# Performance work log

Measured on AMD Instinct MI355X. Metric: run time of the kernel, lower is better.

Reference implementation:

```python
import jax, jax.numpy as jnp
import numpy as np

N_NODES = 50000
NUM_HEAD = 2
NEG_SLOPE_ATT = 0.2
NEG_SLOPE_ACT = 0.3


def _glorot(key, shape):
    fan = shape[-1] + (shape[-2] if len(shape) > 1 else shape[-1])
    lim = jnp.sqrt(6.0 / fan)
    return jax.random.uniform(key, shape, jnp.float32, -lim, lim)


def gat_conv(h, src, dst, W, att, bias):
    # h: (N, in_dim); W: (out_dim, in_dim) torch Linear layout; att: (1, H, 2k)
    N = h.shape[0]
    H = att.shape[1]
    k = att.shape[2] // 2
    x = (h @ W.T).reshape(N, H, k)
    x_i = x[dst]  # target features (E, H, k)
    x_j = x[src]  # source features (E, H, k)
    # alpha = sum(cat([x_i, x_j]) * att) without materializing the concat
    alpha = jnp.einsum('ehk,hk->eh', x_i, att[0, :, :k]) + jnp.einsum('ehk,hk->eh', x_j, att[0, :, k:])
    alpha = jax.nn.leaky_relu(alpha, NEG_SLOPE_ATT)
    # segment softmax grouped by edge_index[0] (src), as in the original code
    m = jax.ops.segment_max(alpha, src, num_segments=N)
    e = jnp.exp(alpha - m[src])
    s = jax.ops.segment_sum(e, src, num_segments=N)
    alpha = e / (s[src] + 1e-16)
    msg = x_j * alpha[:, :, None]
    out = jax.ops.segment_sum(msg, dst, num_segments=N)  # aggregate to targets
    out = out.reshape(N, H * k) + bias
    return jax.nn.relu(out)


def _forward(x, src, dst, node_index, params):
    (W1, att1, b1, W2, att2, b2, W3, att3, b3, W_out, b_out) = params
    h = gat_conv(x, src, dst, W1, att1, b1)
    h = jax.nn.leaky_relu(h, NEG_SLOPE_ACT)
    h = gat_conv(h, src, dst, W2, att2, b2)
    h = jax.nn.leaky_relu(h, NEG_SLOPE_ACT)
    h = gat_conv(h, src, dst, W3, att3, b3)
    x_embed = jax.nn.leaky_relu(h, NEG_SLOPE_ACT)
    output = x_embed @ W_out.T + b_out
    node_output = output[node_index]
    ypred = jnp.argmax(output, axis=1)
    y_nodepred = ypred[node_index]
    return x_embed, node_output, ypred, y_nodepred


def setup_inputs() -> dict:
    key = jax.random.key(0)
    ks = jax.random.split(key, 16)
    N, E, D = N_NODES, 800000, 128
    H, k = NUM_HEAD, 128 // NUM_HEAD
    inp = {
        'x': jax.random.normal(ks[0], (N, D), jnp.float32),
        'edge_index': jax.random.randint(ks[1], (2, E), 0, N, jnp.int64),
        'node_label': jax.random.normal(ks[2], (1000, 1, 3), jnp.float32),
        'node_index': jax.random.randint(ks[3], (1000,), 0, N, jnp.int64),
        'W1': _glorot(ks[4], (D, D)),
        'att1': _glorot(ks[5], (1, H, 2 * k)),
        'b1': jnp.zeros((D,), jnp.float32),
        'W2': _glorot(ks[6], (D, D)),
        'att2': _glorot(ks[7], (1, H, 2 * k)),
        'b2': jnp.zeros((D,), jnp.float32),
        'W3': _glorot(ks[8], (D, D)),
        'att3': _glorot(ks[9], (1, H, 2 * k)),
        'b3': jnp.zeros((D,), jnp.float32),
        'W_out': _glorot(ks[10], (3, D)),
        'b_out': jnp.zeros((3,), jnp.float32),
    }
    return inp


def reference(x, edge_index, node_label, node_index, W1, att1, b1, W2, att2, b2, W3, att3, b3, W_out, b_out):
    N = x.shape[0]
    loop = jnp.arange(N, dtype=edge_index.dtype)
    src = jnp.concatenate([edge_index[0], loop])  # add_self_loops
    dst = jnp.concatenate([edge_index[1], loop])
    params = (W1, att1, b1, W2, att2, b2, W3, att3, b3, W_out, b_out)
    return _forward(x, src, dst, node_index, params)
```

## Files before the change

### kernel.cpp

```cpp
#include <hip/hip_runtime.h>
#include <math.h>


#define EPB 8192

__global__ __launch_bounds__(256) void gemm128(const float* __restrict__ A,
                                               const float* __restrict__ Wm,
                                               const float* __restrict__ att,
                                               float* __restrict__ C,
                                               float4* __restrict__ ni4,
                                               float2* __restrict__ ad2v, int N) {
    __shared__ float As[64][68];
    __shared__ float Wt[64][132];
    const int tx = threadIdx.x;
    const int row0 = blockIdx.x * 64;
    const int cid = tx & 31;
    const int rid = tx >> 5;
    float acc[8][4] = {};
    const float4* A4 = (const float4*)A;
    const float4* W4 = (const float4*)Wm;

    for (int kt = 0; kt < 2; ++kt) {
        for (int i = tx; i < 1024; i += 256) {
            int r = i >> 4, q = i & 15;
            int row = row0 + r;
            float4 v = (row < N) ? A4[(size_t)row * 32 + kt * 16 + q]
                                 : make_float4(0.f, 0.f, 0.f, 0.f);
            As[r][q * 4 + 0] = v.x; As[r][q * 4 + 1] = v.y;
            As[r][q * 4 + 2] = v.z; As[r][q * 4 + 3] = v.w;
        }
        for (int i = tx; i < 2048; i += 256) {
            int c = i >> 4, q = i & 15;
            float4 v = W4[(size_t)c * 32 + kt * 16 + q];
            Wt[q * 4 + 0][c] = v.x; Wt[q * 4 + 1][c] = v.y;
            Wt[q * 4 + 2][c] = v.z; Wt[q * 4 + 3][c] = v.w;
        }
        __syncthreads();
        for (int k = 0; k < 64; k += 4) {
            float4 a[8];
            #pragma unroll
            for (int i = 0; i < 8; ++i) a[i] = *(const float4*)&As[rid * 8 + i][k];
            #pragma unroll
            for (int kk = 0; kk < 4; ++kk) {
                float4 w = *(const float4*)&Wt[k + kk][cid * 4];
                #pragma unroll
                for (int i = 0; i < 8; ++i) {
                    float av = (kk == 0) ? a[i].x : (kk == 1) ? a[i].y : (kk == 2) ? a[i].z : a[i].w;
                    acc[i][0] += av * w.x; acc[i][1] += av * w.y;
                    acc[i][2] += av * w.z; acc[i][3] += av * w.w;
                }
            }
        }
        __syncthreads();
    }
    #pragma unroll
    for (int i = 0; i < 8; ++i) {
        int row = row0 + rid * 8 + i;
        if (row < N)
            ((float4*)C)[(size_t)row * 32 + cid] =
                make_float4(acc[i][0], acc[i][1], acc[i][2], acc[i][3]);
    }
    const int hh = cid >> 4;
    const int c0 = (cid & 15) * 4;
    float ad0 = att[hh * 128 + c0 + 0], ad1 = att[hh * 128 + c0 + 1];
    float ad2c = att[hh * 128 + c0 + 2], ad3 = att[hh * 128 + c0 + 3];
    float as0 = att[hh * 128 + 64 + c0 + 0], as1 = att[hh * 128 + 64 + c0 + 1];
    float as2 = att[hh * 128 + 64 + c0 + 2], as3 = att[hh * 128 + 64 + c0 + 3];
    float pd[8], ps[8];
    #pragma unroll
    for (int i = 0; i < 8; ++i) {
        pd[i] = acc[i][0] * ad0 + acc[i][1] * ad1 + acc[i][2] * ad2c + acc[i][3] * ad3;
        ps[i] = acc[i][0] * as0 + acc[i][1] * as1 + acc[i][2] * as2 + acc[i][3] * as3;
    }
    #pragma unroll
    for (int m = 1; m < 16; m <<= 1) {
        #pragma unroll
        for (int i = 0; i < 8; ++i) {
            pd[i] += __shfl_xor(pd[i], m);
            ps[i] += __shfl_xor(ps[i], m);
        }
    }
    const int ll = tx & 63;
    const int grp = ll & 32;
    #pragma unroll
    for (int i = 0; i < 8; ++i) {
        float d0 = __shfl(pd[i], grp + 0);
        float d1 = __shfl(pd[i], grp + 16);
        float s0 = __shfl(ps[i], grp + 0);
        float s1 = __shfl(ps[i], grp + 16);
        if ((ll & 31) == 0) {
            int row = row0 + rid * 8 + i;
            if (row < N) {
                ad2v[row] = make_float2(d0, d1);
                ni4[row] = make_float4(s0, s1, 0.f, 0.f);
            }
        }
    }
}

__global__ __launch_bounds__(512) void coarse_hist(const int* __restrict__ ei, int E, int Et,
                                                   unsigned int* __restrict__ gh_d,
                                                   unsigned int* __restrict__ gh_s, int CB) {
    __shared__ unsigned int lh_d[800];
    __shared__ unsigned int lh_s[800];
    const int t = threadIdx.x;
    for (int b = t; b < CB; b += 512) { lh_d[b] = 0u; lh_s[b] = 0u; }
    __syncthreads();
    const int i0 = blockIdx.x * EPB;
    for (int i = t; i < EPB; i += 512) {
        int e = i0 + i;
        if (e < Et) {
            int s, d;
            if (e < E) { s = ei[e]; d = ei[E + e]; } else { s = d = e - E; }
            atomicAdd(&lh_d[d >> 6], 1u);
            atomicAdd(&lh_s[s >> 6], 1u);
        }
    }
    __syncthreads();
    for (int b = t; b < CB; b += 512) {
        if (lh_d[b]) atomicAdd(&gh_d[b], lh_d[b]);
        if (lh_s[b]) atomicAdd(&gh_s[b], lh_s[b]);
    }
}

__global__ __launch_bounds__(1024) void coarse_scan(const unsigned int* __restrict__ gh_d,
                                                    const unsigned int* __restrict__ gh_s,
                                                    unsigned int* __restrict__ coff_d,
                                                    unsigned int* __restrict__ coff_s,
                                                    unsigned int* __restrict__ cur_d,
                                                    unsigned int* __restrict__ cur_s,
                                                    int CB, unsigned int total) {
    __shared__ unsigned int sh[1024];
    const int t = threadIdx.x;
    for (int a = 0; a < 2; ++a) {
        const unsigned int* gh = a ? gh_s : gh_d;
        unsigned int* coff = a ? coff_s : coff_d;
        unsigned int* cur  = a ? cur_s : cur_d;
        sh[t] = (t < CB) ? gh[t] : 0u;
        __syncthreads();
        #pragma unroll
        for (int d = 1; d < 1024; d <<= 1) {
            unsigned int u = (t >= d) ? sh[t - d] : 0u;
            __syncthreads();
            sh[t] += u;
            __syncthreads();
        }
        if (t < CB) {
            unsigned int ex = (t == 0) ? 0u : sh[t - 1];
            coff[t] = ex;
            cur[t] = ex;
        }
        if (t == 0) coff[CB] = total;
        __syncthreads();
    }
}

__global__ __launch_bounds__(512) void coarse_scatter_both(const int* __restrict__ ei,
                                                           int E, int Et,
                                                           unsigned int* __restrict__ cur_d,
                                                           unsigned int* __restrict__ cur_s,
                                                           unsigned int* __restrict__ tmp_d,
                                                           unsigned int* __restrict__ tmp_s,
                                                           int CB) {
    __shared__ unsigned int lh_d[800];
    __shared__ unsigned int lh_s[800];
    const int t = threadIdx.x;
    for (int b = t; b < CB; b += 512) { lh_d[b] = 0u; lh_s[b] = 0u; }
    __syncthreads();
    const int i0 = blockIdx.x * EPB;
    for (int i = t; i < EPB; i += 512) {
        int e = i0 + i;
        if (e < Et) {
            int s, d;
            if (e < E) { s = ei[e]; d = ei[E + e]; } else { s = d = e - E; }
            atomicAdd(&lh_d[d >> 6], 1u);
            atomicAdd(&lh_s[s >> 6], 1u);
        }
    }
    __syncthreads();
    for (int b = t; b < CB; b += 512) {
        unsigned int cd = lh_d[b], cs = lh_s[b];
        lh_d[b] = cd ? atomicAdd(&cur_d[b], cd) : 0u;
        lh_s[b] = cs ? atomicAdd(&cur_s[b], cs) : 0u;
    }
    __syncthreads();
    for (int i = t; i < EPB; i += 512) {
        int e = i0 + i;
        if (e < Et) {
            int s, d;
            if (e < E) { s = ei[e]; d = ei[E + e]; } else { s = d = e - E; }
            unsigned int pd = atomicAdd(&lh_d[d >> 6], 1u);
            tmp_d[pd] = ((unsigned int)(d & 63) << 16) | (unsigned int)s;
            unsigned int ps = atomicAdd(&lh_s[s >> 6], 1u);
            tmp_s[ps] = ((unsigned int)(s & 63) << 16) | (unsigned int)d;
        }
    }
}

__global__ __launch_bounds__(256) void fine_sort(const unsigned int* __restrict__ tmp_d,
                                                 const unsigned int* __restrict__ tmp_s,
                                                 const unsigned int* __restrict__ coff_d,
                                                 const unsigned int* __restrict__ coff_s,
                                                 unsigned int* __restrict__ off_d,
                                                 unsigned int* __restrict__ off_s,
                                                 int* __restrict__ srcs,
                                                 int* __restrict__ dsts,
                                                 int N, int CB, unsigned int total) {
    __shared__ unsigned int cnt[64];
    __shared__ unsigned int h[64];
    const bool isS = (int)blockIdx.x >= CB;
    const int b = isS ? (blockIdx.x - CB) : blockIdx.x;
    const unsigned int* tmp  = isS ? tmp_s : tmp_d;
    const unsigned int* coff = isS ? coff_s : coff_d;
    unsigned int* off = isS ? off_s : off_d;
    int* outv = isS ? dsts : srcs;
    const int node0 = b * 64;
    int nn = N - node0; if (nn > 64) nn = 64;
    const int t = threadIdx.x;
    const unsigned int cb0 = coff[b], cb1 = coff[b + 1];
    if (t < 64) cnt[t] = 0u;
    __syncthreads();
    for (unsigned int i = cb0 + t; i < cb1; i += 256)
        atomicAdd(&cnt[tmp[i] >> 16], 1u);
    __syncthreads();
    if (t < 64) h[t] = cnt[t];
    __syncthreads();
    #pragma unroll
    for (int d = 1; d < 64; d <<= 1) {
        unsigned int u = (t < 64 && t >= d) ? h[t - d] : 0u;
        __syncthreads();
        if (t < 64) h[t] += u;
        __syncthreads();
    }
    if (t < 64) h[t] = cb0 + h[t] - cnt[t];
    __syncthreads();
    if (t < nn) off[node0 + t] = h[t];
    if (b == CB - 1 && t == 0) off[N] = total;
    for (unsigned int i = cb0 + t; i < cb1; i += 256) {
        unsigned int v = tmp[i];
        unsigned int pos = atomicAdd(&h[v >> 16], 1u);
        outv[pos] = (int)(v & 0xFFFFu);
    }
}

__global__ __launch_bounds__(256) void src_sum(const int* __restrict__ dsts,
                                               const unsigned int* __restrict__ off_s,
                                               const float2* __restrict__ ad2,
                                               float* __restrict__ ni, int N) {
    int n = blockIdx.x * 256 + threadIdx.x;
    if (n >= N) return;
    float as0 = ni[(size_t)n * 4 + 0];
    float as1 = ni[(size_t)n * 4 + 1];
    unsigned int j0 = off_s[n], j1 = off_s[n + 1];
    float s0 = 0.f, s1 = 0.f;
    unsigned int j = j0;
    for (; j + 4 <= j1; j += 4) {
        int d0 = dsts[j], d1 = dsts[j + 1], d2 = dsts[j + 2], d3 = dsts[j + 3];
        float2 a0 = ad2[d0], a1 = ad2[d1], a2 = ad2[d2], a3 = ad2[d3];
        float t;
        t = as0 + a0.x; t = (t > 0.f) ? t : 0.2f * t; s0 += __expf(t);
        t = as1 + a0.y; t = (t > 0.f) ? t : 0.2f * t; s1 += __expf(t);
        t = as0 + a1.x; t = (t > 0.f) ? t : 0.2f * t; s0 += __expf(t);
        t = as1 + a1.y; t = (t > 0.f) ? t : 0.2f * t; s1 += __expf(t);
        t = as0 + a2.x; t = (t > 0.f) ? t : 0.2f * t; s0 += __expf(t);
        t = as1 + a2.y; t = (t > 0.f) ? t : 0.2f * t; s1 += __expf(t);
        t = as0 + a3.x; t = (t > 0.f) ? t : 0.2f * t; s0 += __expf(t);
        t = as1 + a3.y; t = (t > 0.f) ? t : 0.2f * t; s1 += __expf(t);
    }
    for (; j < j1; ++j) {
        float2 a = ad2[dsts[j]];
        float t;
        t = as0 + a.x; t = (t > 0.f) ? t : 0.2f * t; s0 += __expf(t);
        t = as1 + a.y; t = (t > 0.f) ? t : 0.2f * t; s1 += __expf(t);
    }
    ni[(size_t)n * 4 + 2] = 1.0f / (s0 + 1e-16f);
    ni[(size_t)n * 4 + 3] = 1.0f / (s1 + 1e-16f);
}

__global__ __launch_bounds__(256) void edge_w(const int* __restrict__ srcs,
                                              const unsigned int* __restrict__ off_d,
                                              const float4* __restrict__ ni4,
                                              const float2* __restrict__ ad2,
                                              float2* __restrict__ w2, int N) {
    __shared__ unsigned int lb[65];
    __shared__ float2 lad[64];
    const int node0 = blockIdx.x * 64;
    int nn = N - node0; if (nn > 64) nn = 64;
    const int t = threadIdx.x;
    if (t <= nn) lb[t] = off_d[node0 + t];
    if (t < nn) lad[t] = ad2[node0 + t];
    __syncthreads();
    unsigned int base = lb[0], end = lb[nn];
    for (unsigned int i = base + t; i < end; i += 256) {
        int lo = 0, hi = nn;
        while (hi - lo > 1) {
            int mid = (lo + hi) >> 1;
            if (i >= lb[mid]) lo = mid; else hi = mid;
        }
        float2 ad = lad[lo];
        int s = srcs[i];
        float4 nv = ni4[s];
        float a0 = ad.x + nv.x; a0 = (a0 > 0.f) ? a0 : 0.2f * a0;
        float a1 = ad.y + nv.y; a1 = (a1 > 0.f) ? a1 : 0.2f * a1;
        w2[i] = make_float2(__expf(a0) * nv.z, __expf(a1) * nv.w);
    }
}

template <int U>
__device__ __forceinline__ void agg_edges(unsigned int j, const int* __restrict__ srcs,
                                          const float2* __restrict__ w2,
                                          const float2* __restrict__ x2,
                                          int l, int hi, float& accx, float& accy) {
    int s[U]; float2 w[U]; float2 v[U];
    #pragma unroll
    for (int u = 0; u < U; ++u) s[u] = srcs[j + u];
    #pragma unroll
    for (int u = 0; u < U; ++u) w[u] = w2[j + u];
    #pragma unroll
    for (int u = 0; u < U; ++u) v[u] = x2[(size_t)s[u] * 64 + l];
    #pragma unroll
    for (int u = 0; u < U; ++u) {
        float ww = hi ? w[u].y : w[u].x;
        accx += v[u].x * ww;
        accy += v[u].y * ww;
    }
}

template <bool LAST>
__global__ __launch_bounds__(256) void agg_csr(const int* __restrict__ srcs,
                                               const unsigned int* __restrict__ off,
                                               const float2* __restrict__ x2,
                                               const float2* __restrict__ w2,
                                               const float* __restrict__ bias,
                                               float* __restrict__ out,
                                               const float* __restrict__ Wout,
                                               const float* __restrict__ bout,
                                               float* __restrict__ out3,
                                               float* __restrict__ ypred, int N) {
    int d = blockIdx.x * 4 + (threadIdx.x >> 6);
    int l = threadIdx.x & 63;
    if (d >= N) return;
    d = __builtin_amdgcn_readfirstlane(d);
    const int hi = l >> 5;
    unsigned int j0 = off[d], j1 = off[d + 1];
    float accx = 0.f, accy = 0.f;
    unsigned int j = j0;
    for (; j + 16 <= j1; j += 16) agg_edges<16>(j, srcs, w2, x2, l, hi, accx, accy);
    if (j + 8 <= j1) { agg_edges<8>(j, srcs, w2, x2, l, hi, accx, accy); j += 8; }
    if (j + 4 <= j1) { agg_edges<4>(j, srcs, w2, x2, l, hi, accx, accy); j += 4; }
    if (j + 2 <= j1) { agg_edges<2>(j, srcs, w2, x2, l, hi, accx, accy); j += 2; }
    if (j < j1)      { agg_edges<1>(j, srcs, w2, x2, l, hi, accx, accy); }

    float2 bb = ((const float2*)bias)[l];
    float o0 = fmaxf(accx + bb.x, 0.f);
    float o1 = fmaxf(accy + bb.y, 0.f);
    ((float2*)out)[(size_t)d * 64 + l] = make_float2(o0, o1);
    if (LAST) {
        const float2* W2 = (const float2*)Wout;
        float2 wa = W2[l], wb = W2[64 + l], wc = W2[128 + l];
        float p0 = o0 * wa.x + o1 * wa.y;
        float p1 = o0 * wb.x + o1 * wb.y;
        float p2 = o0 * wc.x + o1 * wc.y;
        #pragma unroll
        for (int m = 32; m; m >>= 1) {
            p0 += __shfl_xor(p0, m);
            p1 += __shfl_xor(p1, m);
            p2 += __shfl_xor(p2, m);
        }
        if (l == 0) {
            p0 += bout[0]; p1 += bout[1]; p2 += bout[2];
            out3[d * 3 + 0] = p0; out3[d * 3 + 1] = p1; out3[d * 3 + 2] = p2;
            int am = 0; float best = p0;
            if (p1 > best) { best = p1; am = 1; }
            if (p2 > best) { best = p2; am = 2; }
            ypred[d] = (float)am;
        }
    }
}

__global__ __launch_bounds__(256) void gather_out(const float* __restrict__ out3,
                                                  const float* __restrict__ ypred,
                                                  const int* __restrict__ node_index,
                                                  float* __restrict__ node_out,
                                                  float* __restrict__ y_nodepred, int M) {
    int i = blockIdx.x * 256 + threadIdx.x;
    if (i >= M) return;
    int idx = node_index[i];
    node_out[i * 3 + 0] = out3[idx * 3 + 0];
    node_out[i * 3 + 1] = out3[idx * 3 + 1];
    node_out[i * 3 + 2] = out3[idx * 3 + 2];
    y_nodepred[i] = ypred[idx];
}

extern "C" void kernel_launch(void* const* d_in, const int* in_sizes, int n_in,
                              void* d_out, int out_size, void* d_ws, size_t ws_size,
                              hipStream_t stream) {
    const float* x          = (const float*)d_in[0];
    const int*   ei         = (const int*)d_in[1];
    const int*   node_index = (const int*)d_in[3];
    const float* W[3]   = {(const float*)d_in[4], (const float*)d_in[7], (const float*)d_in[10]};
    const float* att[3] = {(const float*)d_in[5], (const float*)d_in[8], (const float*)d_in[11]};
    const float* b[3]   = {(const float*)d_in[6], (const float*)d_in[9], (const float*)d_in[12]};
    const float* Wout = (const float*)d_in[13];
    const float* bout = (const float*)d_in[14];

    const int N  = in_sizes[0] / 128;
    const int E  = in_sizes[1] / 2;
    const int Et = E + N;
    const int M  = in_sizes[3];
    const int CB = (N + 63) / 64;
    const int NBLK = (Et + EPB - 1) / EPB;

    float* ws     = (float*)d_ws;
    float* xlin   = ws;
    unsigned int* tmp_d = (unsigned int*)ws;
    unsigned int* tmp_s = tmp_d + (size_t)Et;
    float* hb     = xlin + (size_t)N * 128;
    float* ad     = hb + (size_t)N * 128;
    float* ni     = ad + (size_t)N * 2;
    float* out3   = ad;
    unsigned int* off_d = (unsigned int*)(ni + (size_t)N * 4);
    unsigned int* off_s = off_d + (size_t)N + 4;
    unsigned int* gh_d  = off_s + (size_t)N + 4;
    unsigned int* gh_s  = gh_d + 1024;
    unsigned int* coff_d = gh_s + 1024;
    unsigned int* coff_s = coff_d + 1024;
    unsigned int* cur_d  = coff_s + 1024;
    unsigned int* cur_s  = cur_d + 1024;
    int* srcs = (int*)(cur_s + 1024);
    int* dsts = srcs + (size_t)Et;
    float2* w2 = (float2*)(dsts + (size_t)Et);

    float* o_embed = (float*)d_out;
    float* o_node  = o_embed + (size_t)N * 128;
    float* o_ypred = o_node + (size_t)M * 3;
    float* o_ynode = o_ypred + (size_t)N;

    const int gemm_blocks = (N + 63) / 64;
    const int node_wave_blocks = (N + 3) / 4;
    const int n_blocks = (N + 255) / 256;

    hipMemsetAsync(gh_d, 0, 2048 * sizeof(unsigned int), stream);
    coarse_hist<<<NBLK, 512, 0, stream>>>(ei, E, Et, gh_d, gh_s, CB);
    coarse_scan<<<1, 1024, 0, stream>>>(gh_d, gh_s, coff_d, coff_s, cur_d, cur_s,
                                        CB, (unsigned int)Et);
    coarse_scatter_both<<<NBLK, 512, 0, stream>>>(ei, E, Et, cur_d, cur_s, tmp_d, tmp_s, CB);
    fine_sort<<<2 * CB, 256, 0, stream>>>(tmp_d, tmp_s, coff_d, coff_s, off_d, off_s,
                                          srcs, dsts, N, CB, (unsigned int)Et);

    for (int L = 0; L < 3; ++L) {
        const float* hin = (L == 0) ? x : hb;
        gemm128<<<gemm_blocks, 256, 0, stream>>>(hin, W[L], att[L], xlin,
                                                 (float4*)ni, (float2*)ad, N);
        src_sum<<<n_blocks, 256, 0, stream>>>(dsts, off_s, (const float2*)ad, ni, N);
        edge_w<<<CB, 256, 0, stream>>>(srcs, off_d, (const float4*)ni, (const float2*)ad,
                                       w2, N);
        if (L < 2)
            agg_csr<false><<<node_wave_blocks, 256, 0, stream>>>(
                srcs, off_d, (const float2*)xlin, (const float2*)w2,
                b[L], hb, nullptr, nullptr, nullptr, nullptr, N);
        else
            agg_csr<true><<<node_wave_blocks, 256, 0, stream>>>(
                srcs, off_d, (const float2*)xlin, (const float2*)w2,
                b[L], o_embed, Wout, bout, out3, o_ypred, N);
    }
    gather_out<<<(M + 255) / 256, 256, 0, stream>>>(out3, o_ypred, node_index, o_node, o_ynode, M);
}
```

Baseline: 419.3 us.

## Replace fp32 SIMT GEMM with split-bf16 MFMA GEMM emulating fp32 precision

Splits weights (in a small pre-kernel) and activations (on load) into three bf16 parts and computes the 128x128 node projection with bf16 MFMA instructions using six cross-term products. The attention dot products are reduced via shuffles and shared memory. This aims to move the GEMM from FMA units to matrix cores, at the cost of large LDS use (single block per CU), extra conversion work and an extra launch per layer.

```diff
diff --git a/kernel.cpp b/kernel.cpp
--- a/kernel.cpp
+++ b/kernel.cpp
@@ -4,96 +4,172 @@
 
 #define EPB 8192
 
-__global__ __launch_bounds__(256) void gemm128(const float* __restrict__ A,
-                                               const float* __restrict__ Wm,
-                                               const float* __restrict__ att,
-                                               float* __restrict__ C,
-                                               float4* __restrict__ ni4,
-                                               float2* __restrict__ ad2v, int N) {
-    __shared__ float As[64][68];
-    __shared__ float Wt[64][132];
+typedef __attribute__((ext_vector_type(8))) short short8v;
+typedef __attribute__((ext_vector_type(4))) short short4v;
+typedef __attribute__((ext_vector_type(4))) float f32x4;
+
+__global__ __launch_bounds__(256) void wsplit(const float* __restrict__ Wm,
+                                              unsigned short* __restrict__ Wb) {
+    int i = blockIdx.x * 256 + threadIdx.x;
+    if (i >= 16384) return;
+    float v = Wm[i];
+    unsigned int u = __float_as_uint(v);
+    unsigned int h1 = (u + 0x7FFFu + ((u >> 16) & 1u)) >> 16;
+    float r = v - __uint_as_float(h1 << 16);
+    unsigned int u2 = __float_as_uint(r);
+    unsigned int h2 = (u2 + 0x7FFFu + ((u2 >> 16) & 1u)) >> 16;
+    float r2 = r - __uint_as_float(h2 << 16);
+    unsigned int u3 = __float_as_uint(r2);
+    unsigned int h3 = (u3 + 0x7FFFu + ((u3 >> 16) & 1u)) >> 16;
+    Wb[i] = (unsigned short)h1;
+    Wb[16384 + i] = (unsigned short)h2;
+    Wb[32768 + i] = (unsigned short)h3;
+}
+
+#define APL 8704
+#define WPL 16896
+__global__ __launch_bounds__(256) void gemm_mfma(const float* __restrict__ A,
+                                                 const unsigned short* __restrict__ Wb,
+                                                 const float* __restrict__ att,
+                                                 float* __restrict__ C,
+                                                 float4* __restrict__ ni4,
+                                                 float2* __restrict__ ad2v, int N) {
+    __shared__ unsigned short AL[3 * APL];
+    __shared__ unsigned short WL[3 * WPL];
+    __shared__ float SR[4][64][2];
     const int tx = threadIdx.x;
     const int row0 = blockIdx.x * 64;
-    const int cid = tx & 31;
-    const int rid = tx >> 5;
-    float acc[8][4] = {};
     const float4* A4 = (const float4*)A;
-    const float4* W4 = (const float4*)Wm;
-
-    for (int kt = 0; kt < 2; ++kt) {
-        for (int i = tx; i < 1024; i += 256) {
-            int r = i >> 4, q = i & 15;
-            int row = row0 + r;
-            float4 v = (row < N) ? A4[(size_t)row * 32 + kt * 16 + q]
-                                 : make_float4(0.f, 0.f, 0.f, 0.f);
-            As[r][q * 4 + 0] = v.x; As[r][q * 4 + 1] = v.y;
-            As[r][q * 4 + 2] = v.z; As[r][q * 4 + 3] = v.w;
-        }
-        for (int i = tx; i < 2048; i += 256) {
-            int c = i >> 4, q = i & 15;
-            float4 v = W4[(size_t)c * 32 + kt * 16 + q];
-            Wt[q * 4 + 0][c] = v.x; Wt[q * 4 + 1][c] = v.y;
-            Wt[q * 4 + 2][c] = v.z; Wt[q * 4 + 3][c] = v.w;
-        }
-        __syncthreads();
-        for (int k = 0; k < 64; k += 4) {
-            float4 a[8];
+
+    for (int i = tx; i < 2048; i += 256) {
+        int r = i >> 5, q = i & 31;
+        int row = row0 + r;
+        float4 v = (row < N) ? A4[(size_t)row * 32 + q] : make_float4(0.f, 0.f, 0.f, 0.f);
+        float e[4] = {v.x, v.y, v.z, v.w};
+        unsigned int h1[4], h2[4], h3[4];
+        #pragma unroll
+        for (int j = 0; j < 4; ++j) {
+            unsigned int u = __float_as_uint(e[j]);
+            h1[j] = (u + 0x7FFFu + ((u >> 16) & 1u)) >> 16;
+            float r1 = e[j] - __uint_as_float(h1[j] << 16);
+            unsigned int u2 = __float_as_uint(r1);
+            h2[j] = (u2 + 0x7FFFu + ((u2 >> 16) & 1u)) >> 16;
+            float r2 = r1 - __uint_as_float(h2[j] << 16);
+            unsigned int u3 = __float_as_uint(r2);
+            h3[j] = (u3 + 0x7FFFu + ((u3 >> 16) & 1u)) >> 16;
+        }
+        int base = r * 136 + q * 4;
+        *(uint2*)&AL[0 * APL + base] = make_uint2(h1[0] | (h1[1] << 16), h1[2] | (h1[3] << 16));
+        *(uint2*)&AL[1 * APL + base] = make_uint2(h2[0] | (h2[1] << 16), h2[2] | (h2[3] << 16));
+        *(uint2*)&AL[2 * APL + base] = make_uint2(h3[0] | (h3[1] << 16), h3[2] | (h3[3] << 16));
+    }
+    for (int i = tx; i < 12288; i += 256) {
+        int p = i >> 12, rem = i & 4095;
+        int col = rem >> 5, q = rem & 31;
+        uint2 v = ((const uint2*)Wb)[i];
+        *(uint2*)&WL[p * WPL + col * 132 + q * 4] = v;
+    }
+    __syncthreads();
+
+    const int lane = tx & 63;
+    const int wid = tx >> 6;
+    const int cl = lane & 15;
+    const int kg = lane >> 4;
+
+    f32x4 acc[2][4];
+    #pragma unroll
+    for (int cc = 0; cc < 2; ++cc)
+        #pragma unroll
+        for (int rt = 0; rt < 4; ++rt)
+            acc[cc][rt] = (f32x4){0.f, 0.f, 0.f, 0.f};
+
+    for (int kk = 0; kk < 4; ++kk) {
+        short8v af[4][3];
+        #pragma unroll
+        for (int rt = 0; rt < 4; ++rt)
             #pragma unroll
-            for (int i = 0; i < 8; ++i) a[i] = *(const float4*)&As[rid * 8 + i][k];
+            for (int p = 0; p < 3; ++p)
+                af[rt][p] = *(const short8v*)&AL[p * APL + (rt * 16 + cl) * 136 + kk * 32 + kg * 8];
+        short8v bfr[2][3];
+        #pragma unroll
+        for (int cc = 0; cc < 2; ++cc) {
+            int col = wid * 32 + cc * 16 + cl;
             #pragma unroll
-            for (int kk = 0; kk < 4; ++kk) {
-                float4 w = *(const float4*)&Wt[k + kk][cid * 4];
-                #pragma unroll
-                for (int i = 0; i < 8; ++i) {
-                    float av = (kk == 0) ? a[i].x : (kk == 1) ? a[i].y : (kk == 2) ? a[i].z : a[i].w;
-                    acc[i][0] += av * w.x; acc[i][1] += av * w.y;
-                    acc[i][2] += av * w.z; acc[i][3] += av * w.w;
-                }
+            for (int p = 0; p < 3; ++p) {
+                int base = p * WPL + col * 132 + kk * 32 + kg * 8;
+                short4v b0 = *(const short4v*)&WL[base];
+                short4v b1 = *(const short4v*)&WL[base + 4];
+                short8v b;
+                b[0] = b0[0]; b[1] = b0[1]; b[2] = b0[2]; b[3] = b0[3];
+                b[4] = b1[0]; b[5] = b1[1]; b[6] = b1[2]; b[7] = b1[3];
+                bfr[cc][p] = b;
             }
         }
-        __syncthreads();
-    }
-    #pragma unroll
-    for (int i = 0; i < 8; ++i) {
-        int row = row0 + rid * 8 + i;
-        if (row < N)
-            ((float4*)C)[(size_t)row * 32 + cid] =
-                make_float4(acc[i][0], acc[i][1], acc[i][2], acc[i][3]);
-    }
-    const int hh = cid >> 4;
-    const int c0 = (cid & 15) * 4;
-    float ad0 = att[hh * 128 + c0 + 0], ad1 = att[hh * 128 + c0 + 1];
-    float ad2c = att[hh * 128 + c0 + 2], ad3 = att[hh * 128 + c0 + 3];
-    float as0 = att[hh * 128 + 64 + c0 + 0], as1 = att[hh * 128 + 64 + c0 + 1];
-    float as2 = att[hh * 128 + 64 + c0 + 2], as3 = att[hh * 128 + 64 + c0 + 3];
-    float pd[8], ps[8];
-    #pragma unroll
-    for (int i = 0; i < 8; ++i) {
-        pd[i] = acc[i][0] * ad0 + acc[i][1] * ad1 + acc[i][2] * ad2c + acc[i][3] * ad3;
-        ps[i] = acc[i][0] * as0 + acc[i][1] * as1 + acc[i][2] * as2 + acc[i][3] * as3;
-    }
-    #pragma unroll
-    for (int m = 1; m < 16; m <<= 1) {
-        #pragma unroll
-        for (int i = 0; i < 8; ++i) {
-            pd[i] += __shfl_xor(pd[i], m);
-            ps[i] += __shfl_xor(ps[i], m);
-        }
-    }
-    const int ll = tx & 63;
-    const int grp = ll & 32;
-    #pragma unroll
-    for (int i = 0; i < 8; ++i) {
-        float d0 = __shfl(pd[i], grp + 0);
-        float d1 = __shfl(pd[i], grp + 16);
-        float s0 = __shfl(ps[i], grp + 0);
-        float s1 = __shfl(ps[i], grp + 16);
-        if ((ll & 31) == 0) {
-            int row = row0 + rid * 8 + i;
-            if (row < N) {
-                ad2v[row] = make_float2(d0, d1);
-                ni4[row] = make_float4(s0, s1, 0.f, 0.f);
+        #pragma unroll
+        for (int cc = 0; cc < 2; ++cc)
+            #pragma unroll
+            for (int rt = 0; rt < 4; ++rt) {
+                f32x4 a = acc[cc][rt];
+                a = __builtin_amdgcn_mfma_f32_16x16x32_bf16(af[rt][0], bfr[cc][0], a, 0, 0, 0);
+                a = __builtin_amdgcn_mfma_f32_16x16x32_bf16(af[rt][0], bfr[cc][1], a, 0, 0, 0);
+                a = __builtin_amdgcn_mfma_f32_16x16x32_bf16(af[rt][1], bfr[cc][0], a, 0, 0, 0);
+                a = __builtin_amdgcn_mfma_f32_16x16x32_bf16(af[rt][0], bfr[cc][2], a, 0, 0, 0);
+                a = __builtin_amdgcn_mfma_f32_16x16x32_bf16(af[rt][1], bfr[cc][1], a, 0, 0, 0);
+                a = __builtin_amdgcn_mfma_f32_16x16x32_bf16(af[rt][2], bfr[cc][0], a, 0, 0, 0);
+                acc[cc][rt] = a;
             }
+    }
+
+    #pragma unroll
+    for (int cc = 0; cc < 2; ++cc)
+        #pragma unroll
+        for (int rt = 0; rt < 4; ++rt)
+            #pragma unroll
+            for (int r = 0; r < 4; ++r) {
+                int row = row0 + rt * 16 + kg * 4 + r;
+                if (row < N) C[(size_t)row * 128 + wid * 32 + cc * 16 + cl] = acc[cc][rt][r];
+            }
+
+    const int hh = wid >> 1;
+    float attd0 = att[hh * 128 + (wid & 1) * 32 + cl];
+    float attd1 = att[hh * 128 + (wid & 1) * 32 + 16 + cl];
+    float atts0 = att[hh * 128 + 64 + (wid & 1) * 32 + cl];
+    float atts1 = att[hh * 128 + 64 + (wid & 1) * 32 + 16 + cl];
+    #pragma unroll
+    for (int rt = 0; rt < 4; ++rt) {
+        float pd[4], ps[4];
+        #pragma unroll
+        for (int r = 0; r < 4; ++r) {
+            pd[r] = acc[0][rt][r] * attd0 + acc[1][rt][r] * attd1;
+            ps[r] = acc[0][rt][r] * atts0 + acc[1][rt][r] * atts1;
+        }
+        #pragma unroll
+        for (int m = 1; m < 16; m <<= 1) {
+            #pragma unroll
+            for (int r = 0; r < 4; ++r) {
+                pd[r] += __shfl_xor(pd[r], m);
+                ps[r] += __shfl_xor(ps[r], m);
+            }
+        }
+        if (cl == 0) {
+            #pragma unroll
+            for (int r = 0; r < 4; ++r) {
+                int rl = rt * 16 + kg * 4 + r;
+                SR[wid][rl][0] = pd[r];
+                SR[wid][rl][1] = ps[r];
+            }
+        }
+    }
+    __syncthreads();
+    if (tx < 64) {
+        int row = row0 + tx;
+        if (row < N) {
+            float pd0 = SR[0][tx][0] + SR[1][tx][0];
+            float ps0 = SR[0][tx][1] + SR[1][tx][1];
+            float pd1 = SR[2][tx][0] + SR[3][tx][0];
+            float ps1 = SR[2][tx][1] + SR[3][tx][1];
+            ad2v[row] = make_float2(pd0, pd1);
+            ni4[row] = make_float4(ps0, ps1, 0.f, 0.f);
         }
     }
 }
@@ -430,6 +506,7 @@
     int* srcs = (int*)(cur_s + 1024);
     int* dsts = srcs + (size_t)Et;
     float2* w2 = (float2*)(dsts + (size_t)Et);
+    unsigned short* Wb = (unsigned short*)(w2 + (size_t)Et);
 
     float* o_embed = (float*)d_out;
     float* o_node  = o_embed + (size_t)N * 128;
@@ -450,8 +527,9 @@
 
     for (int L = 0; L < 3; ++L) {
         const float* hin = (L == 0) ? x : hb;
-        gemm128<<<gemm_blocks, 256, 0, stream>>>(hin, W[L], att[L], xlin,
-                                                 (float4*)ni, (float2*)ad, N);
+        wsplit<<<64, 256, 0, stream>>>(W[L], Wb);
+        gemm_mfma<<<gemm_blocks, 256, 0, stream>>>(hin, Wb, att[L], xlin,
+                                                   (float4*)ni, (float2*)ad, N);
         src_sum<<<n_blocks, 256, 0, stream>>>(dsts, off_s, (const float2*)ad, ni, N);
         edge_w<<<CB, 256, 0, stream>>>(srcs, off_d, (const float4*)ni, (const float2*)ad,
                                        w2, N);
```

Measured after the change: 490.2 us. +16.9%, slower.
